# Kernel optimization log

Measured on AMD Instinct MI355X. Metric: run time of the kernel, lower is better.

Reference implementation:

```python
import jax, jax.numpy as jnp
import numpy as np

NU = 0.01 / np.pi  # Burgers viscosity
LAYERS = [2, 128, 128, 128, 128, 1]
N_EQ, N_INIT, N_BND = 131072, 4096, 4096


def setup_inputs() -> dict:
    key = jax.random.key(0)
    ks = jax.random.split(key, 16)
    inp = {
        'tx_equation': jax.random.uniform(ks[0], (N_EQ, 2), dtype=jnp.float32),
        'tx_init': jax.random.uniform(ks[1], (N_INIT, 2), dtype=jnp.float32),
        'tx_bound': jax.random.uniform(ks[2], (N_BND, 2), dtype=jnp.float32),
    }
    # Glorot-normal initialized Dense weights, zero biases (keras defaults in build_network)
    for i, (fin, fout) in enumerate(zip(LAYERS[:-1], LAYERS[1:])):
        std = np.sqrt(2.0 / (fin + fout)).astype(np.float32)
        inp[f'W{i}'] = jax.random.normal(ks[3 + i], (fin, fout), dtype=jnp.float32) * std
        inp[f'b{i}'] = jnp.zeros((fout,), dtype=jnp.float32)
    return inp


def _mlp_scalar(tx, Ws, bs):
    # tx: (2,) -> scalar u. tanh hidden layers, linear output.
    h = tx
    for W, b in zip(Ws[:-1], bs[:-1]):
        h = jnp.tanh(h @ W + b)
    return (h @ Ws[-1] + bs[-1])[0]


def reference(tx_equation, tx_init, tx_bound, W0, b0, W1, b1, W2, b2, W3, b3, W4, b4):
    Ws = [W0, W1, W2, W3, W4]
    bs = [b0, b1, b2, b3, b4]

    def u_s(tx):
        return _mlp_scalar(tx, Ws, bs)

    def u_x_s(tx):
        return jax.grad(u_s)(tx)[1]

    # PDE residual on collocation points
    u = jax.vmap(u_s)(tx_equation)                     # (N,)
    g = jax.vmap(jax.grad(u_s))(tx_equation)           # (N, 2) -> columns (u_t, u_x)
    u_t, u_x = g[:, 0], g[:, 1]
    u_xx = jax.vmap(jax.grad(u_x_s))(tx_equation)[:, 1]  # (N,)
    burgers_eq = (u_t + u * u_x - NU * u_xx)[:, None]     # (N, 1)

    # Initial / boundary predictions (single fused batch like tf.concat in call)
    tx_ib = jnp.concatenate([tx_init, tx_bound], axis=0)
    u_ib = jax.vmap(u_s)(tx_ib)[:, None]
    n_i = tx_init.shape[0]
    return burgers_eq, u_ib[:n_i], u_ib[n_i:]
```

## Files before the change

kernel.cpp:

```cpp
#include <hip/hip_runtime.h>
#include <math.h>

#define NU_F 0.0031830988618379067f
#define HS 136

typedef __attribute__((ext_vector_type(8))) _Float16 half8;
typedef __attribute__((ext_vector_type(4))) _Float16 half4;
typedef __attribute__((ext_vector_type(16))) float f32x16;

__device__ __forceinline__ float fast_tanh(float x) {
    const float e = __builtin_amdgcn_exp2f(x * 2.8853900817779268f);
    const float r = __builtin_amdgcn_rcpf(e + 1.f);
    return fmaf(-2.f, r, 1.f);
}

__global__ void prep_kernel(const float* __restrict__ W1,
                            const float* __restrict__ W2,
                            const float* __restrict__ W3,
                            _Float16* __restrict__ ws)
{
    const int g = blockIdx.x * 256 + threadIdx.x;
    const int l = g >> 14;
    const int r = g & 16383;
    const int n = r & 127;
    const int k = r >> 7;
    const float* W = (l == 0) ? W1 : (l == 1) ? W2 : W3;
    const float w = W[k * 128 + n];
    ws[l * 16384 + (k >> 4) * 2048 + n * 16 + (k & 15)] = (_Float16)w;
}

__launch_bounds__(256, 4)
__global__ void pinn_kernel(const float* __restrict__ tx_eq,
                            const float* __restrict__ tx_init,
                            const float* __restrict__ tx_bnd,
                            const float* __restrict__ W0, const float* __restrict__ b0,
                            const float* __restrict__ b1, const float* __restrict__ b2,
                            const float* __restrict__ b3,
                            const float* __restrict__ W4, const float* __restrict__ b4,
                            const _Float16* __restrict__ wt,
                            float* __restrict__ out)
{
    __shared__ _Float16 Hh[128][HS];

    const int tid   = threadIdx.x;
    const int blk   = blockIdx.x;
    const bool is_eq = (blk < 4096);
    const int w     = tid >> 6;
    const int lane  = tid & 63;
    const int col   = lane & 31;
    const int khalf = lane >> 5;
    const int ncol  = 32 * w + col;
    const int wofs  = ncol * 16 + khalf * 8;

    if (is_eq) {
        const int p  = tid >> 3;
        const int f0 = (tid & 7) * 16;
        const float tv = tx_eq[blk * 64 + 2 * p];
        const float xv = tx_eq[blk * 64 + 2 * p + 1];
        const int m0 = 4 * p;
        #pragma unroll
        for (int half = 0; half < 2; ++half) {
            const int fb = f0 + 8 * half;
            float vch[4][8];
            #pragma unroll
            for (int j = 0; j < 8; ++j) {
                const int f = fb + j;
                const float w0v = W0[f];
                const float w1v = W0[128 + f];
                const float z = fmaf(tv, w0v, fmaf(xv, w1v, b0[f]));
                const float a = fast_tanh(z);
                const float s = 1.f - a * a;
                vch[0][j] = a;
                vch[1][j] = s * w0v;
                vch[2][j] = s * w1v;
                vch[3][j] = -2.f * a * s * w1v * w1v;
            }
            #pragma unroll
            for (int c = 0; c < 4; ++c) {
                half8 hh;
                #pragma unroll
                for (int j = 0; j < 8; ++j) hh[j] = (_Float16)vch[c][j];
                *(half8*)&Hh[m0 + c][fb] = hh;
            }
        }
    } else {
        const int p  = tid >> 1;
        const int f0 = (tid & 1) * 64;
        const int gp = (blk - 4096) * 128 + p;
        const float* src = (gp < 4096) ? tx_init : tx_bnd;
        const int idx = (gp < 4096) ? gp : gp - 4096;
        const float tv = src[2 * idx];
        const float xv = src[2 * idx + 1];
        #pragma unroll
        for (int g = 0; g < 8; ++g) {
            half8 hh;
            #pragma unroll
            for (int j = 0; j < 8; ++j) {
                const int f = f0 + 8 * g + j;
                hh[j] = (_Float16)fast_tanh(fmaf(tv, W0[f], fmaf(xv, W0[128 + f], b0[f])));
            }
            *(half8*)&Hh[p][f0 + 8 * g] = hh;
        }
    }
    __syncthreads();

    const float* barr[3] = {b1, b2, b3};

    #pragma unroll 1
    for (int layer = 0; layer < 3; ++layer) {
        const _Float16* __restrict__ ph = wt + layer * 16384 + wofs;
        const float bias = barr[layer][ncol];

        half8 q0 = *(const half8*)(ph);
        half8 q1 = *(const half8*)(ph + 2048);
        half8 q2 = *(const half8*)(ph + 4096);
        half8 q3 = *(const half8*)(ph + 6144);
        half8 q4 = *(const half8*)(ph + 8192);
        half8 q5 = *(const half8*)(ph + 10240);
        half8 q6 = *(const half8*)(ph + 12288);
        half8 q7 = *(const half8*)(ph + 14336);

        f32x16 acc0, acc1, acc2, acc3;
        #pragma unroll
        for (int e = 0; e < 16; ++e) {
            acc0[e] = 0.f; acc1[e] = 0.f; acc2[e] = 0.f; acc3[e] = 0.f;
        }

#define KSTEP(KT, Q)                                                          \
        {                                                                     \
            const int k0 = KT * 16 + khalf * 8;                               \
            const half8 ah0 = *(const half8*)&Hh[col][k0];                    \
            const half8 ah1 = *(const half8*)&Hh[32 + col][k0];               \
            const half8 ah2 = *(const half8*)&Hh[64 + col][k0];               \
            const half8 ah3 = *(const half8*)&Hh[96 + col][k0];               \
            acc0 = __builtin_amdgcn_mfma_f32_32x32x16_f16(ah0, Q, acc0, 0, 0, 0); \
            acc1 = __builtin_amdgcn_mfma_f32_32x32x16_f16(ah1, Q, acc1, 0, 0, 0); \
            acc2 = __builtin_amdgcn_mfma_f32_32x32x16_f16(ah2, Q, acc2, 0, 0, 0); \
            acc3 = __builtin_amdgcn_mfma_f32_32x32x16_f16(ah3, Q, acc3, 0, 0, 0); \
        }
        KSTEP(0, q0) KSTEP(1, q1) KSTEP(2, q2) KSTEP(3, q3)
        KSTEP(4, q4) KSTEP(5, q5) KSTEP(6, q6) KSTEP(7, q7)
#undef KSTEP

        half4 h16[4][4];
        #pragma unroll
        for (int mt = 0; mt < 4; ++mt)
            #pragma unroll
            for (int g = 0; g < 4; ++g) {
                const float A0 = (mt == 0 ? acc0 : mt == 1 ? acc1 : mt == 2 ? acc2 : acc3)[4 * g + 0];
                const float A1 = (mt == 0 ? acc0 : mt == 1 ? acc1 : mt == 2 ? acc2 : acc3)[4 * g + 1];
                const float A2 = (mt == 0 ? acc0 : mt == 1 ? acc1 : mt == 2 ? acc2 : acc3)[4 * g + 2];
                const float A3 = (mt == 0 ? acc0 : mt == 1 ? acc1 : mt == 2 ? acc2 : acc3)[4 * g + 3];
                half4 hv;
                if (is_eq) {
                    const float t = fast_tanh(A0 + bias);
                    const float s = 1.f - t * t;
                    hv[0] = (_Float16)t;
                    hv[1] = (_Float16)(s * A1);
                    hv[2] = (_Float16)(s * A2);
                    hv[3] = (_Float16)fmaf(s, A3, -2.f * t * s * A2 * A2);
                } else {
                    hv[0] = (_Float16)fast_tanh(A0 + bias);
                    hv[1] = (_Float16)fast_tanh(A1 + bias);
                    hv[2] = (_Float16)fast_tanh(A2 + bias);
                    hv[3] = (_Float16)fast_tanh(A3 + bias);
                }
                h16[mt][g] = hv;
            }

        __syncthreads();

        #pragma unroll
        for (int mt = 0; mt < 4; ++mt)
            #pragma unroll
            for (int g = 0; g < 4; ++g) {
                const int mrow0 = mt * 32 + 8 * g + 4 * khalf;
                Hh[mrow0 + 0][ncol] = h16[mt][g][0];
                Hh[mrow0 + 1][ncol] = h16[mt][g][1];
                Hh[mrow0 + 2][ncol] = h16[mt][g][2];
                Hh[mrow0 + 3][ncol] = h16[mt][g][3];
            }
        __syncthreads();
    }

    {
        const float b4v = b4[0];
        const int m = tid >> 1;
        const int q = tid & 1;
        float dot = 0.f;
        #pragma unroll
        for (int g = 0; g < 8; ++g) {
            const int f = 64 * q + 8 * g;
            const half8 hh = *(const half8*)&Hh[m][f];
            const float4 wa = *(const float4*)&W4[f];
            const float4 wb = *(const float4*)&W4[f + 4];
            dot = fmaf((float)hh[0], wa.x, dot);
            dot = fmaf((float)hh[1], wa.y, dot);
            dot = fmaf((float)hh[2], wa.z, dot);
            dot = fmaf((float)hh[3], wa.w, dot);
            dot = fmaf((float)hh[4], wb.x, dot);
            dot = fmaf((float)hh[5], wb.y, dot);
            dot = fmaf((float)hh[6], wb.z, dot);
            dot = fmaf((float)hh[7], wb.w, dot);
        }
        dot += __shfl_xor(dot, 1);

        if (is_eq) {
            const int base = (lane & 7) * 8;
            const float uu   = __shfl(dot, base + 0) + b4v;
            const float utv  = __shfl(dot, base + 2);
            const float uxv  = __shfl(dot, base + 4);
            const float uxxv = __shfl(dot, base + 6);
            if (lane < 8)
                out[blk * 32 + 8 * w + lane] = fmaf(uu, uxv, utv) - NU_F * uxxv;
        } else {
            if (q == 0)
                out[131072 + (blk - 4096) * 128 + m] = dot + b4v;
        }
    }
}

extern "C" void kernel_launch(void* const* d_in, const int* in_sizes, int n_in,
                              void* d_out, int out_size, void* d_ws, size_t ws_size,
                              hipStream_t stream)
{
    const float* tx_eq   = (const float*)d_in[0];
    const float* tx_init = (const float*)d_in[1];
    const float* tx_bnd  = (const float*)d_in[2];
    const float* W0 = (const float*)d_in[3];
    const float* b0 = (const float*)d_in[4];
    const float* W1 = (const float*)d_in[5];
    const float* b1 = (const float*)d_in[6];
    const float* W2 = (const float*)d_in[7];
    const float* b2 = (const float*)d_in[8];
    const float* W3 = (const float*)d_in[9];
    const float* b3 = (const float*)d_in[10];
    const float* W4 = (const float*)d_in[11];
    const float* b4 = (const float*)d_in[12];
    float* out = (float*)d_out;
    _Float16* wt = (_Float16*)d_ws;

    hipLaunchKernelGGL(prep_kernel, dim3(192), dim3(256), 0, stream, W1, W2, W3, wt);
    hipLaunchKernelGGL(pinn_kernel, dim3(4160), dim3(256), 0, stream,
                       tx_eq, tx_init, tx_bnd, W0, b0, b1, b2, b3, W4, b4,
                       (const _Float16*)wt, out);
}
```

Before: 167.0 us.

## Halve rows per block to cut accumulators and raise occupancy

Each block now handles 64 MLP rows instead of 128 (16 collocation points with their 4 derivative channels), so each wave keeps two MFMA accumulators instead of four. The LDS tile halves, the grid doubles, and launch bounds ask for 5 blocks per CU so more waves can hide latency. The bias is folded into the accumulator initialisation, applied only to the value channel for equation rows, and the output reduction is remapped to 4 threads per row. In exchange, every block reloads the same per-layer weight fragments for half as much MFMA work, and there are more blocks and barriers in total.

```diff
diff --git a/kernel.cpp b/kernel.cpp
--- a/kernel.cpp
+++ b/kernel.cpp
@@ -29,7 +29,7 @@
     ws[l * 16384 + (k >> 4) * 2048 + n * 16 + (k & 15)] = (_Float16)w;
 }
 
-__launch_bounds__(256, 4)
+__launch_bounds__(256, 5)
 __global__ void pinn_kernel(const float* __restrict__ tx_eq,
                             const float* __restrict__ tx_init,
                             const float* __restrict__ tx_bnd,
@@ -40,11 +40,11 @@
                             const _Float16* __restrict__ wt,
                             float* __restrict__ out)
 {
-    __shared__ _Float16 Hh[128][HS];
+    __shared__ _Float16 Hh[64][HS];
 
     const int tid   = threadIdx.x;
     const int blk   = blockIdx.x;
-    const bool is_eq = (blk < 4096);
+    const bool is_eq = (blk < 8192);
     const int w     = tid >> 6;
     const int lane  = tid & 63;
     const int col   = lane & 31;
@@ -53,46 +53,42 @@
     const int wofs  = ncol * 16 + khalf * 8;
 
     if (is_eq) {
-        const int p  = tid >> 3;
-        const int f0 = (tid & 7) * 16;
-        const float tv = tx_eq[blk * 64 + 2 * p];
-        const float xv = tx_eq[blk * 64 + 2 * p + 1];
+        const int p  = tid >> 4;
+        const int fb = (tid & 15) * 8;
+        const float tv = tx_eq[blk * 32 + 2 * p];
+        const float xv = tx_eq[blk * 32 + 2 * p + 1];
         const int m0 = 4 * p;
-        #pragma unroll
-        for (int half = 0; half < 2; ++half) {
-            const int fb = f0 + 8 * half;
-            float vch[4][8];
-            #pragma unroll
-            for (int j = 0; j < 8; ++j) {
-                const int f = fb + j;
-                const float w0v = W0[f];
-                const float w1v = W0[128 + f];
-                const float z = fmaf(tv, w0v, fmaf(xv, w1v, b0[f]));
-                const float a = fast_tanh(z);
-                const float s = 1.f - a * a;
-                vch[0][j] = a;
-                vch[1][j] = s * w0v;
-                vch[2][j] = s * w1v;
-                vch[3][j] = -2.f * a * s * w1v * w1v;
-            }
-            #pragma unroll
-            for (int c = 0; c < 4; ++c) {
-                half8 hh;
-                #pragma unroll
-                for (int j = 0; j < 8; ++j) hh[j] = (_Float16)vch[c][j];
-                *(half8*)&Hh[m0 + c][fb] = hh;
-            }
+        float vch[4][8];
+        #pragma unroll
+        for (int j = 0; j < 8; ++j) {
+            const int f = fb + j;
+            const float w0v = W0[f];
+            const float w1v = W0[128 + f];
+            const float z = fmaf(tv, w0v, fmaf(xv, w1v, b0[f]));
+            const float a = fast_tanh(z);
+            const float s = 1.f - a * a;
+            vch[0][j] = a;
+            vch[1][j] = s * w0v;
+            vch[2][j] = s * w1v;
+            vch[3][j] = -2.f * a * s * w1v * w1v;
+        }
+        #pragma unroll
+        for (int c = 0; c < 4; ++c) {
+            half8 hh;
+            #pragma unroll
+            for (int j = 0; j < 8; ++j) hh[j] = (_Float16)vch[c][j];
+            *(half8*)&Hh[m0 + c][fb] = hh;
         }
     } else {
-        const int p  = tid >> 1;
-        const int f0 = (tid & 1) * 64;
-        const int gp = (blk - 4096) * 128 + p;
+        const int p  = tid >> 2;
+        const int f0 = (tid & 3) * 32;
+        const int gp = (blk - 8192) * 64 + p;
         const float* src = (gp < 4096) ? tx_init : tx_bnd;
         const int idx = (gp < 4096) ? gp : gp - 4096;
         const float tv = src[2 * idx];
         const float xv = src[2 * idx + 1];
         #pragma unroll
-        for (int g = 0; g < 8; ++g) {
+        for (int g = 0; g < 4; ++g) {
             half8 hh;
             #pragma unroll
             for (int j = 0; j < 8; ++j) {
@@ -120,10 +116,11 @@
         half8 q6 = *(const half8*)(ph + 12288);
         half8 q7 = *(const half8*)(ph + 14336);
 
-        f32x16 acc0, acc1, acc2, acc3;
+        f32x16 acc0, acc1;
         #pragma unroll
         for (int e = 0; e < 16; ++e) {
-            acc0[e] = 0.f; acc1[e] = 0.f; acc2[e] = 0.f; acc3[e] = 0.f;
+            const float v = (is_eq && (e & 3) != 0) ? 0.f : bias;
+            acc0[e] = v; acc1[e] = v;
         }
 
 #define KSTEP(KT, Q)                                                          \
@@ -131,39 +128,35 @@
             const int k0 = KT * 16 + khalf * 8;                               \
             const half8 ah0 = *(const half8*)&Hh[col][k0];                    \
             const half8 ah1 = *(const half8*)&Hh[32 + col][k0];               \
-            const half8 ah2 = *(const half8*)&Hh[64 + col][k0];               \
-            const half8 ah3 = *(const half8*)&Hh[96 + col][k0];               \
             acc0 = __builtin_amdgcn_mfma_f32_32x32x16_f16(ah0, Q, acc0, 0, 0, 0); \
             acc1 = __builtin_amdgcn_mfma_f32_32x32x16_f16(ah1, Q, acc1, 0, 0, 0); \
-            acc2 = __builtin_amdgcn_mfma_f32_32x32x16_f16(ah2, Q, acc2, 0, 0, 0); \
-            acc3 = __builtin_amdgcn_mfma_f32_32x32x16_f16(ah3, Q, acc3, 0, 0, 0); \
         }
         KSTEP(0, q0) KSTEP(1, q1) KSTEP(2, q2) KSTEP(3, q3)
         KSTEP(4, q4) KSTEP(5, q5) KSTEP(6, q6) KSTEP(7, q7)
 #undef KSTEP
 
-        half4 h16[4][4];
-        #pragma unroll
-        for (int mt = 0; mt < 4; ++mt)
+        half4 h16[2][4];
+        #pragma unroll
+        for (int mt = 0; mt < 2; ++mt)
             #pragma unroll
             for (int g = 0; g < 4; ++g) {
-                const float A0 = (mt == 0 ? acc0 : mt == 1 ? acc1 : mt == 2 ? acc2 : acc3)[4 * g + 0];
-                const float A1 = (mt == 0 ? acc0 : mt == 1 ? acc1 : mt == 2 ? acc2 : acc3)[4 * g + 1];
-                const float A2 = (mt == 0 ? acc0 : mt == 1 ? acc1 : mt == 2 ? acc2 : acc3)[4 * g + 2];
-                const float A3 = (mt == 0 ? acc0 : mt == 1 ? acc1 : mt == 2 ? acc2 : acc3)[4 * g + 3];
+                const float A0 = (mt == 0 ? acc0 : acc1)[4 * g + 0];
+                const float A1 = (mt == 0 ? acc0 : acc1)[4 * g + 1];
+                const float A2 = (mt == 0 ? acc0 : acc1)[4 * g + 2];
+                const float A3 = (mt == 0 ? acc0 : acc1)[4 * g + 3];
                 half4 hv;
                 if (is_eq) {
-                    const float t = fast_tanh(A0 + bias);
+                    const float t = fast_tanh(A0);
                     const float s = 1.f - t * t;
                     hv[0] = (_Float16)t;
                     hv[1] = (_Float16)(s * A1);
                     hv[2] = (_Float16)(s * A2);
                     hv[3] = (_Float16)fmaf(s, A3, -2.f * t * s * A2 * A2);
                 } else {
-                    hv[0] = (_Float16)fast_tanh(A0 + bias);
-                    hv[1] = (_Float16)fast_tanh(A1 + bias);
-                    hv[2] = (_Float16)fast_tanh(A2 + bias);
-                    hv[3] = (_Float16)fast_tanh(A3 + bias);
+                    hv[0] = (_Float16)fast_tanh(A0);
+                    hv[1] = (_Float16)fast_tanh(A1);
+                    hv[2] = (_Float16)fast_tanh(A2);
+                    hv[3] = (_Float16)fast_tanh(A3);
                 }
                 h16[mt][g] = hv;
             }
@@ -171,7 +164,7 @@
         __syncthreads();
 
         #pragma unroll
-        for (int mt = 0; mt < 4; ++mt)
+        for (int mt = 0; mt < 2; ++mt)
             #pragma unroll
             for (int g = 0; g < 4; ++g) {
                 const int mrow0 = mt * 32 + 8 * g + 4 * khalf;
@@ -185,12 +178,12 @@
 
     {
         const float b4v = b4[0];
-        const int m = tid >> 1;
-        const int q = tid & 1;
+        const int m = tid >> 2;
+        const int q = tid & 3;
         float dot = 0.f;
         #pragma unroll
-        for (int g = 0; g < 8; ++g) {
-            const int f = 64 * q + 8 * g;
+        for (int g = 0; g < 4; ++g) {
+            const int f = 32 * q + 8 * g;
             const half8 hh = *(const half8*)&Hh[m][f];
             const float4 wa = *(const float4*)&W4[f];
             const float4 wb = *(const float4*)&W4[f + 4];
@@ -204,18 +197,20 @@
             dot = fmaf((float)hh[7], wb.w, dot);
         }
         dot += __shfl_xor(dot, 1);
+        dot += __shfl_xor(dot, 2);
 
         if (is_eq) {
-            const int base = (lane & 7) * 8;
+            const int j = lane >> 4;
+            const int base = 16 * j;
             const float uu   = __shfl(dot, base + 0) + b4v;
-            const float utv  = __shfl(dot, base + 2);
-            const float uxv  = __shfl(dot, base + 4);
-            const float uxxv = __shfl(dot, base + 6);
-            if (lane < 8)
-                out[blk * 32 + 8 * w + lane] = fmaf(uu, uxv, utv) - NU_F * uxxv;
+            const float utv  = __shfl(dot, base + 4);
+            const float uxv  = __shfl(dot, base + 8);
+            const float uxxv = __shfl(dot, base + 12);
+            if ((lane & 15) == 0)
+                out[blk * 16 + 4 * w + j] = fmaf(uu, uxv, utv) - NU_F * uxxv;
         } else {
             if (q == 0)
-                out[131072 + (blk - 4096) * 128 + m] = dot + b4v;
+                out[131072 + (blk - 8192) * 64 + m] = dot + b4v;
         }
     }
 }
@@ -241,7 +236,7 @@
     _Float16* wt = (_Float16*)d_ws;
 
     hipLaunchKernelGGL(prep_kernel, dim3(192), dim3(256), 0, stream, W1, W2, W3, wt);
-    hipLaunchKernelGGL(pinn_kernel, dim3(4160), dim3(256), 0, stream,
+    hipLaunchKernelGGL(pinn_kernel, dim3(8320), dim3(256), 0, stream,
                        tx_eq, tx_init, tx_bnd, W0, b0, b1, b2, b3, W4, b4,
                        (const _Float16*)wt, out);
 }
```

New measurement: 171.1 us. 1.02x slower.

## Keep activations in registers via transposed MFMA, dropping LDS round-trips

Applied to the files above, without the earlier changes.

The hidden-layer GEMMs are restructured so each wave computes W^T·H with weights as the A operand and activations as the B operand. The MFMA output layout then matches the next layer's B-operand layout, so activations stay in registers and the shared-memory tile, barriers and scattered LDS stores are removed. The forward-mode derivative channels are exchanged between neighbouring lanes with DPP quad broadcasts, and biases are folded into the accumulator init. Weights are repacked into lane-fragment order and loaded from global or L2 on every k-step, and the occupancy hint drops from 4 to 3 to leave room for the extra registers.

```diff
diff --git a/kernel.cpp b/kernel.cpp
--- a/kernel.cpp
+++ b/kernel.cpp
@@ -2,16 +2,37 @@
 #include <math.h>
 
 #define NU_F 0.0031830988618379067f
-#define HS 136
 
 typedef __attribute__((ext_vector_type(8))) _Float16 half8;
-typedef __attribute__((ext_vector_type(4))) _Float16 half4;
 typedef __attribute__((ext_vector_type(16))) float f32x16;
 
 __device__ __forceinline__ float fast_tanh(float x) {
     const float e = __builtin_amdgcn_exp2f(x * 2.8853900817779268f);
     const float r = __builtin_amdgcn_rcpf(e + 1.f);
     return fmaf(-2.f, r, 1.f);
+}
+
+__device__ __forceinline__ uint32_t pack2(float x, float y) {
+    union { _Float16 h[2]; uint32_t u; } r;
+    r.h[0] = (_Float16)x; r.h[1] = (_Float16)y;
+    return r.u;
+}
+
+__device__ __forceinline__ half8 pack8(const float* v) {
+    union { uint32_t u[4]; half8 h; } r;
+    r.u[0] = pack2(v[0], v[1]);
+    r.u[1] = pack2(v[2], v[3]);
+    r.u[2] = pack2(v[4], v[5]);
+    r.u[3] = pack2(v[6], v[7]);
+    return r.h;
+}
+
+template<int CTRL>
+__device__ __forceinline__ float qb(float v) {
+    union { float f; int i; } a, b;
+    a.f = v;
+    b.i = __builtin_amdgcn_update_dpp(0, a.i, CTRL, 0xF, 0xF, true);
+    return b.f;
 }
 
 __global__ void prep_kernel(const float* __restrict__ W1,
@@ -20,16 +41,19 @@
                             _Float16* __restrict__ ws)
 {
     const int g = blockIdx.x * 256 + threadIdx.x;
-    const int l = g >> 14;
-    const int r = g & 16383;
-    const int n = r & 127;
-    const int k = r >> 7;
+    const int j    = g & 7;
+    const int lane = (g >> 3) & 63;
+    const int tn   = (g >> 9) & 3;
+    const int kt   = (g >> 11) & 7;
+    const int l    = g >> 14;
+    const int h    = lane >> 5;
+    const int n    = 32 * tn + (lane & 31);
+    const int k    = 32 * (kt >> 1) + 16 * (kt & 1) + 4 * h + (j & 3) + 8 * (j >> 2);
     const float* W = (l == 0) ? W1 : (l == 1) ? W2 : W3;
-    const float w = W[k * 128 + n];
-    ws[l * 16384 + (k >> 4) * 2048 + n * 16 + (k & 15)] = (_Float16)w;
-}
-
-__launch_bounds__(256, 4)
+    ws[g] = (_Float16)W[k * 128 + n];
+}
+
+__launch_bounds__(256, 3)
 __global__ void pinn_kernel(const float* __restrict__ tx_eq,
                             const float* __restrict__ tx_init,
                             const float* __restrict__ tx_bnd,
@@ -40,183 +64,144 @@
                             const _Float16* __restrict__ wt,
                             float* __restrict__ out)
 {
-    __shared__ _Float16 Hh[128][HS];
-
-    const int tid   = threadIdx.x;
-    const int blk   = blockIdx.x;
+    const int tid = threadIdx.x;
+    const int blk = blockIdx.x;
     const bool is_eq = (blk < 4096);
-    const int w     = tid >> 6;
-    const int lane  = tid & 63;
-    const int col   = lane & 31;
-    const int khalf = lane >> 5;
-    const int ncol  = 32 * w + col;
-    const int wofs  = ncol * 16 + khalf * 8;
-
+    const int w    = tid >> 6;
+    const int lane = tid & 63;
+    const int lr   = lane & 31;
+    const int h    = lane >> 5;
+    const int c    = lr & 3;
+    const int h4   = 4 * h;
+
+    float tv, xv;
     if (is_eq) {
-        const int p  = tid >> 3;
-        const int f0 = (tid & 7) * 16;
-        const float tv = tx_eq[blk * 64 + 2 * p];
-        const float xv = tx_eq[blk * 64 + 2 * p + 1];
-        const int m0 = 4 * p;
-        #pragma unroll
-        for (int half = 0; half < 2; ++half) {
-            const int fb = f0 + 8 * half;
-            float vch[4][8];
+        const float2 t2 = ((const float2*)tx_eq)[blk * 32 + 8 * w + (lr >> 2)];
+        tv = t2.x; xv = t2.y;
+    } else {
+        const int gp = (blk - 4096) * 128 + 32 * w + lr;
+        const float2* src = (gp < 4096) ? (const float2*)tx_init : (const float2*)tx_bnd;
+        const float2 t2 = src[(gp < 4096) ? gp : gp - 4096];
+        tv = t2.x; xv = t2.y;
+    }
+    const float bm = (is_eq && c != 0) ? 0.f : 1.f;
+
+    half8 ph[8];
+    #pragma unroll
+    for (int t = 0; t < 4; ++t) {
+        float v16[16];
+        #pragma unroll
+        for (int q = 0; q < 4; ++q) {
+            const int f0 = 32 * t + 8 * q + h4;
+            const float4 w0c = *(const float4*)&W0[f0];
+            const float4 w1c = *(const float4*)&W0[128 + f0];
+            const float4 b0c = *(const float4*)&b0[f0];
             #pragma unroll
-            for (int j = 0; j < 8; ++j) {
-                const int f = fb + j;
-                const float w0v = W0[f];
-                const float w1v = W0[128 + f];
-                const float z = fmaf(tv, w0v, fmaf(xv, w1v, b0[f]));
+            for (int e = 0; e < 4; ++e) {
+                const float w0v = (e == 0) ? w0c.x : (e == 1) ? w0c.y : (e == 2) ? w0c.z : w0c.w;
+                const float w1v = (e == 0) ? w1c.x : (e == 1) ? w1c.y : (e == 2) ? w1c.z : w1c.w;
+                const float b0v = (e == 0) ? b0c.x : (e == 1) ? b0c.y : (e == 2) ? b0c.z : b0c.w;
+                const float z = fmaf(tv, w0v, fmaf(xv, w1v, b0v));
                 const float a = fast_tanh(z);
-                const float s = 1.f - a * a;
-                vch[0][j] = a;
-                vch[1][j] = s * w0v;
-                vch[2][j] = s * w1v;
-                vch[3][j] = -2.f * a * s * w1v * w1v;
-            }
+                float o = a;
+                if (is_eq) {
+                    const float s = 1.f - a * a;
+                    const float v1 = s * w0v;
+                    const float v2 = s * w1v;
+                    const float v3 = -2.f * a * s * w1v * w1v;
+                    o = (c == 0) ? a : (c == 1) ? v1 : (c == 2) ? v2 : v3;
+                }
+                v16[4 * q + e] = o;
+            }
+        }
+        ph[2 * t]     = pack8(&v16[0]);
+        ph[2 * t + 1] = pack8(&v16[8]);
+    }
+
+    const float* barr[3] = {b1, b2, b3};
+    const _Float16* pw = wt;
+    float dot = 0.f;
+
+    #pragma unroll 1
+    for (int l = 0; l < 3; ++l) {
+        const float* __restrict__ bl = barr[l];
+
+        f32x16 acc[4];
+        #pragma unroll
+        for (int t = 0; t < 4; ++t)
             #pragma unroll
-            for (int c = 0; c < 4; ++c) {
-                half8 hh;
+            for (int q = 0; q < 4; ++q) {
+                const float4 bc = *(const float4*)&bl[32 * t + 8 * q + h4];
+                acc[t][4 * q + 0] = bc.x * bm;
+                acc[t][4 * q + 1] = bc.y * bm;
+                acc[t][4 * q + 2] = bc.z * bm;
+                acc[t][4 * q + 3] = bc.w * bm;
+            }
+
+        #pragma unroll
+        for (int kt = 0; kt < 8; ++kt) {
+            const _Float16* pb = pw + kt * 2048 + lane * 8;
+            const half8 wf0 = *(const half8*)(pb);
+            const half8 wf1 = *(const half8*)(pb + 512);
+            const half8 wf2 = *(const half8*)(pb + 1024);
+            const half8 wf3 = *(const half8*)(pb + 1536);
+            acc[0] = __builtin_amdgcn_mfma_f32_32x32x16_f16(wf0, ph[kt], acc[0], 0, 0, 0);
+            acc[1] = __builtin_amdgcn_mfma_f32_32x32x16_f16(wf1, ph[kt], acc[1], 0, 0, 0);
+            acc[2] = __builtin_amdgcn_mfma_f32_32x32x16_f16(wf2, ph[kt], acc[2], 0, 0, 0);
+            acc[3] = __builtin_amdgcn_mfma_f32_32x32x16_f16(wf3, ph[kt], acc[3], 0, 0, 0);
+        }
+        pw += 16384;
+
+        const bool last = (l == 2);
+        #pragma unroll
+        for (int t = 0; t < 4; ++t) {
+            float v16[16];
+            #pragma unroll
+            for (int r = 0; r < 16; ++r) {
+                const float z = acc[t][r];
+                float o;
+                if (is_eq) {
+                    const float z0 = qb<0x00>(z);
+                    const float z2 = qb<0xAA>(z);
+                    const float tt = fast_tanh(z0);
+                    const float s  = 1.f - tt * tt;
+                    const float v12 = s * z;
+                    const float m3  = tt * s * z2;
+                    const float v3  = fmaf(s, z, -2.f * m3 * z2);
+                    o = (c == 0) ? tt : (c == 3) ? v3 : v12;
+                } else {
+                    o = fast_tanh(z);
+                }
+                v16[r] = o;
+            }
+            if (last) {
                 #pragma unroll
-                for (int j = 0; j < 8; ++j) hh[j] = (_Float16)vch[c][j];
-                *(half8*)&Hh[m0 + c][fb] = hh;
+                for (int q = 0; q < 4; ++q) {
+                    const float4 w4c = *(const float4*)&W4[32 * t + 8 * q + h4];
+                    dot = fmaf(v16[4 * q + 0], w4c.x, dot);
+                    dot = fmaf(v16[4 * q + 1], w4c.y, dot);
+                    dot = fmaf(v16[4 * q + 2], w4c.z, dot);
+                    dot = fmaf(v16[4 * q + 3], w4c.w, dot);
+                }
+            } else {
+                ph[2 * t]     = pack8(&v16[0]);
+                ph[2 * t + 1] = pack8(&v16[8]);
             }
         }
+    }
+
+    dot += __shfl_xor(dot, 32);
+    const float b4v = b4[0];
+    if (is_eq) {
+        const float u   = qb<0x00>(dot) + b4v;
+        const float ut  = qb<0x55>(dot);
+        const float ux  = qb<0xAA>(dot);
+        const float uxx = qb<0xFF>(dot);
+        if (lane < 32 && c == 0)
+            out[blk * 32 + 8 * w + (lr >> 2)] = fmaf(u, ux, ut) - NU_F * uxx;
     } else {
-        const int p  = tid >> 1;
-        const int f0 = (tid & 1) * 64;
-        const int gp = (blk - 4096) * 128 + p;
-        const float* src = (gp < 4096) ? tx_init : tx_bnd;
-        const int idx = (gp < 4096) ? gp : gp - 4096;
-        const float tv = src[2 * idx];
-        const float xv = src[2 * idx + 1];
-        #pragma unroll
-        for (int g = 0; g < 8; ++g) {
-            half8 hh;
-            #pragma unroll
-            for (int j = 0; j < 8; ++j) {
-                const int f = f0 + 8 * g + j;
-                hh[j] = (_Float16)fast_tanh(fmaf(tv, W0[f], fmaf(xv, W0[128 + f], b0[f])));
-            }
-            *(half8*)&Hh[p][f0 + 8 * g] = hh;
-        }
-    }
-    __syncthreads();
-
-    const float* barr[3] = {b1, b2, b3};
-
-    #pragma unroll 1
-    for (int layer = 0; layer < 3; ++layer) {
-        const _Float16* __restrict__ ph = wt + layer * 16384 + wofs;
-        const float bias = barr[layer][ncol];
-
-        half8 q0 = *(const half8*)(ph);
-        half8 q1 = *(const half8*)(ph + 2048);
-        half8 q2 = *(const half8*)(ph + 4096);
-        half8 q3 = *(const half8*)(ph + 6144);
-        half8 q4 = *(const half8*)(ph + 8192);
-        half8 q5 = *(const half8*)(ph + 10240);
-        half8 q6 = *(const half8*)(ph + 12288);
-        half8 q7 = *(const half8*)(ph + 14336);
-
-        f32x16 acc0, acc1, acc2, acc3;
-        #pragma unroll
-        for (int e = 0; e < 16; ++e) {
-            acc0[e] = 0.f; acc1[e] = 0.f; acc2[e] = 0.f; acc3[e] = 0.f;
-        }
-
-#define KSTEP(KT, Q)                                                          \
-        {                                                                     \
-            const int k0 = KT * 16 + khalf * 8;                               \
-            const half8 ah0 = *(const half8*)&Hh[col][k0];                    \
-            const half8 ah1 = *(const half8*)&Hh[32 + col][k0];               \
-            const half8 ah2 = *(const half8*)&Hh[64 + col][k0];               \
-            const half8 ah3 = *(const half8*)&Hh[96 + col][k0];               \
-            acc0 = __builtin_amdgcn_mfma_f32_32x32x16_f16(ah0, Q, acc0, 0, 0, 0); \
-            acc1 = __builtin_amdgcn_mfma_f32_32x32x16_f16(ah1, Q, acc1, 0, 0, 0); \
-            acc2 = __builtin_amdgcn_mfma_f32_32x32x16_f16(ah2, Q, acc2, 0, 0, 0); \
-            acc3 = __builtin_amdgcn_mfma_f32_32x32x16_f16(ah3, Q, acc3, 0, 0, 0); \
-        }
-        KSTEP(0, q0) KSTEP(1, q1) KSTEP(2, q2) KSTEP(3, q3)
-        KSTEP(4, q4) KSTEP(5, q5) KSTEP(6, q6) KSTEP(7, q7)
-#undef KSTEP
-
-        half4 h16[4][4];
-        #pragma unroll
-        for (int mt = 0; mt < 4; ++mt)
-            #pragma unroll
-            for (int g = 0; g < 4; ++g) {
-                const float A0 = (mt == 0 ? acc0 : mt == 1 ? acc1 : mt == 2 ? acc2 : acc3)[4 * g + 0];
-                const float A1 = (mt == 0 ? acc0 : mt == 1 ? acc1 : mt == 2 ? acc2 : acc3)[4 * g + 1];
-                const float A2 = (mt == 0 ? acc0 : mt == 1 ? acc1 : mt == 2 ? acc2 : acc3)[4 * g + 2];
-                const float A3 = (mt == 0 ? acc0 : mt == 1 ? acc1 : mt == 2 ? acc2 : acc3)[4 * g + 3];
-                half4 hv;
-                if (is_eq) {
-                    const float t = fast_tanh(A0 + bias);
-                    const float s = 1.f - t * t;
-                    hv[0] = (_Float16)t;
-                    hv[1] = (_Float16)(s * A1);
-                    hv[2] = (_Float16)(s * A2);
-                    hv[3] = (_Float16)fmaf(s, A3, -2.f * t * s * A2 * A2);
-                } else {
-                    hv[0] = (_Float16)fast_tanh(A0 + bias);
-                    hv[1] = (_Float16)fast_tanh(A1 + bias);
-                    hv[2] = (_Float16)fast_tanh(A2 + bias);
-                    hv[3] = (_Float16)fast_tanh(A3 + bias);
-                }
-                h16[mt][g] = hv;
-            }
-
-        __syncthreads();
-
-        #pragma unroll
-        for (int mt = 0; mt < 4; ++mt)
-            #pragma unroll
-            for (int g = 0; g < 4; ++g) {
-                const int mrow0 = mt * 32 + 8 * g + 4 * khalf;
-                Hh[mrow0 + 0][ncol] = h16[mt][g][0];
-                Hh[mrow0 + 1][ncol] = h16[mt][g][1];
-                Hh[mrow0 + 2][ncol] = h16[mt][g][2];
-                Hh[mrow0 + 3][ncol] = h16[mt][g][3];
-            }
-        __syncthreads();
-    }
-
-    {
-        const float b4v = b4[0];
-        const int m = tid >> 1;
-        const int q = tid & 1;
-        float dot = 0.f;
-        #pragma unroll
-        for (int g = 0; g < 8; ++g) {
-            const int f = 64 * q + 8 * g;
-            const half8 hh = *(const half8*)&Hh[m][f];
-            const float4 wa = *(const float4*)&W4[f];
-            const float4 wb = *(const float4*)&W4[f + 4];
-            dot = fmaf((float)hh[0], wa.x, dot);
-            dot = fmaf((float)hh[1], wa.y, dot);
-            dot = fmaf((float)hh[2], wa.z, dot);
-            dot = fmaf((float)hh[3], wa.w, dot);
-            dot = fmaf((float)hh[4], wb.x, dot);
-            dot = fmaf((float)hh[5], wb.y, dot);
-            dot = fmaf((float)hh[6], wb.z, dot);
-            dot = fmaf((float)hh[7], wb.w, dot);
-        }
-        dot += __shfl_xor(dot, 1);
-
-        if (is_eq) {
-            const int base = (lane & 7) * 8;
-            const float uu   = __shfl(dot, base + 0) + b4v;
-            const float utv  = __shfl(dot, base + 2);
-            const float uxv  = __shfl(dot, base + 4);
-            const float uxxv = __shfl(dot, base + 6);
-            if (lane < 8)
-                out[blk * 32 + 8 * w + lane] = fmaf(uu, uxv, utv) - NU_F * uxxv;
-        } else {
-            if (q == 0)
-                out[131072 + (blk - 4096) * 128 + m] = dot + b4v;
-        }
+        if (lane < 32)
+            out[131072 + (blk - 4096) * 128 + 32 * w + lr] = dot + b4v;
     }
 }
 
```

Measured after the change: 272.6 us. 63.3% more time.
